# Kernel tuning notes

Measured on AMD Instinct MI355X. Metric: run time of the kernel, lower is better.

Reference implementation:

```python
import jax, jax.numpy as jnp
import numpy as np

N_NODES = 50_000
N_EDGES = 1_600_000
IN_HIDDEN = 256
OUT_HIDDEN = 32
EDGE_HIDDEN = 64
NHEAD = 4
N_EDGE_TYPES = 8
NEG_SLOPE = 0.2


def _glorot(key, shape):
    stdv = np.sqrt(6.0 / (shape[-2] + shape[-1]))
    return jax.random.uniform(key, shape, jnp.float32, -stdv, stdv)


def setup_inputs() -> dict:
    key = jax.random.key(0)
    ks = jax.random.split(key, 10)
    src = jax.random.randint(ks[0], (N_EDGES,), 0, N_NODES, dtype=jnp.int32)
    trg = jax.random.randint(ks[1], (N_EDGES,), 0, N_NODES, dtype=jnp.int32)
    etype = jax.random.randint(ks[2], (N_EDGES,), 0, N_EDGE_TYPES, dtype=jnp.int32)
    edge = jnp.stack([src, trg, etype], axis=0)  # [3, E]
    x = jax.random.normal(ks[3], (N_NODES, IN_HIDDEN), jnp.float32)
    return {
        "edge": edge,
        "x": x,
        "edge_emb": _glorot(ks[4], (N_EDGE_TYPES, EDGE_HIDDEN)),
        "W": _glorot(ks[5], (IN_HIDDEN, OUT_HIDDEN * NHEAD)),
        "W_e": _glorot(ks[6], (EDGE_HIDDEN, EDGE_HIDDEN * NHEAD)),
        "a_l": _glorot(ks[7], (1, NHEAD, OUT_HIDDEN)),
        "a_r": _glorot(ks[8], (1, NHEAD, OUT_HIDDEN)),
        "a_e": _glorot(ks[9], (1, NHEAD, EDGE_HIDDEN)),
    }


def reference(edge, x, edge_emb, W, W_e, a_l, a_r, a_e):
    num_nodes = x.shape[0]
    src, trg, etype = edge[0], edge[1], edge[2]

    # node / edge-type projections
    h = (x @ W).reshape(num_nodes, NHEAD, OUT_HIDDEN)          # [N, H, D]
    h = jnp.where(jnp.isnan(h), 0.0, h)
    e = (edge_emb @ W_e).reshape(N_EDGE_TYPES, NHEAD, EDGE_HIDDEN)  # [T, H, De]

    # per-node / per-type attention logits, gathered to edges -> [E, H]
    h_l = (a_l * h).sum(-1)[src]
    h_r = (a_r * h).sum(-1)[trg]
    h_e = (a_e * e).sum(-1)[etype]
    scores = jax.nn.leaky_relu(h_l + h_r + h_e, NEG_SLOPE)     # [E, H]

    # neighborhood-aware softmax (global max shift, as in original)
    exp_scores = jnp.exp(scores - jnp.max(scores))
    denom = jax.ops.segment_sum(exp_scores, trg, num_segments=num_nodes)  # [N, H]
    attn = (exp_scores / (denom[trg] + 1e-16))[:, :, None]     # [E, H, 1]

    # weighted aggregation: scatter-add messages to targets
    msgs = h[src] * attn                                       # [E, H, D]
    out = jax.ops.segment_sum(msgs, trg, num_segments=num_nodes)  # [N, H, D]
    return out, attn
```

## Files before the change

### kernel.cpp

```cpp
#include <hip/hip_runtime.h>
#include <hip/hip_bf16.h>
#include <hip/hip_fp16.h>

#define N_NODES 50000
#define N_EDGES 1600000
#define IN_H 256
#define NHEAD 4
#define EDGE_H 64
#define N_ET 8


typedef __attribute__((ext_vector_type(8))) short bf16x8v;
typedef __attribute__((ext_vector_type(4))) float f32x4;

__device__ __forceinline__ float ldT(const float* p) { return *p; }
__device__ __forceinline__ float ldT(const __hip_bfloat16* p) { return __bfloat162float(*p); }
__device__ __forceinline__ void stT(float* p, float v) { *p = v; }
__device__ __forceinline__ void stT(__hip_bfloat16* p, float v) { *p = __float2bfloat16(v); }

__device__ __forceinline__ short f2bs(float f) {
    __hip_bfloat16 b = __float2bfloat16(f);
    return (short)__builtin_bit_cast(unsigned short, b);
}
__device__ __forceinline__ float bs2f(short s) {
    return __uint_as_float(((unsigned)(unsigned short)s) << 16);
}

__device__ __forceinline__ unsigned enc_f32(float f) {
    unsigned u = __float_as_uint(f);
    return (u & 0x80000000u) ? ~u : (u | 0x80000000u);
}
__device__ __forceinline__ float dec_f32(unsigned u) {
    return __uint_as_float((u & 0x80000000u) ? (u & 0x7fffffffu) : ~u);
}
__device__ __forceinline__ float lrelu(float v) { return v > 0.f ? v : 0.2f * v; }

__device__ __forceinline__ unsigned pack_h2(float a, float b) {
    unsigned lo = (unsigned)__half_as_ushort(__float2half(a));
    unsigned hi = (unsigned)__half_as_ushort(__float2half(b));
    return lo | (hi << 16);
}
__device__ __forceinline__ float2 unpack_h2(int w) {
    __half2 h = __builtin_bit_cast(__half2, w);
    return __half22float2(h);
}

__global__ void k_detect(const unsigned* __restrict__ xw, int* __restrict__ flag) {
    int lane = threadIdx.x;
    int cnt = 0;
    for (int i = lane; i < 1024; i += 64) {
        unsigned e = (xw[i] >> 23) & 255u;
        if (e >= 64u && e <= 160u) cnt++;
    }
    for (int off = 32; off; off >>= 1) cnt += __shfl_xor(cnt, off);
    if (lane == 0) *flag = (cnt > 512) ? 1 : 0;
}

template<typename T, int EXPECT>
__global__ __launch_bounds__(256) void k_setup(
        const void* __restrict__ Wv, const void* __restrict__ embv,
        const void* __restrict__ Wev, const void* __restrict__ aev,
        __hip_bfloat16* __restrict__ Wt, float* __restrict__ h_e,
        unsigned* __restrict__ hemax, const int* __restrict__ flag) {
    if (*flag != EXPECT) return;
    const T* W   = (const T*)Wv;
    const T* emb = (const T*)embv;
    const T* We  = (const T*)Wev;
    const T* ae  = (const T*)aev;
    if (blockIdx.x == 0) {
        for (int i = threadIdx.x; i < 128 * 256; i += 256) {
            int c = i >> 8, k = i & 255;
            Wt[i] = __float2bfloat16(ldT(W + k * 128 + c));
        }
        return;
    }
    int ty = blockIdx.x - 1;
    int t = threadIdx.x, lane = t & 63;
    float acc = 0.f;
    for (int k = 0; k < EDGE_H; ++k)
        acc += ldT(emb + ty * EDGE_H + k) * ldT(We + k * 256 + t);
    float v = ldT(ae + t) * acc;
    for (int off = 32; off; off >>= 1) v += __shfl_xor(v, off);
    if (lane == 0) {
        h_e[ty * NHEAD + (t >> 6)] = v;
        atomicMax(&hemax[t >> 6], enc_f32(v));
    }
}

template<typename T, int EXPECT>
__global__ __launch_bounds__(256) void k_proj(const void* __restrict__ xv,
        const __hip_bfloat16* __restrict__ Wt, __hip_bfloat16* __restrict__ h,
        float* __restrict__ hl, float* __restrict__ hr,
        const void* __restrict__ alv, const void* __restrict__ arv,
        const int* __restrict__ edge, int* __restrict__ counts,
        const int* __restrict__ flag) {
    if (*flag != EXPECT) return;
    {
        int base = blockIdx.x * 1024;
        int lim = min(base + 1024, N_EDGES);
        for (int i = base + threadIdx.x; i < lim; i += 256)
            atomicAdd(&counts[edge[N_EDGES + i]], 1);
    }
    const T* x  = (const T*)xv;
    const T* al = (const T*)alv;
    const T* ar = (const T*)arv;
    int wid = threadIdx.x >> 6, lane = threadIdx.x & 63;
    int rg = blockIdx.x * 2 + (wid >> 1);
    if (rg >= 3125) return;
    int toff = (wid & 1) * 4;
    int r0 = rg * 16;
    int r = lane & 15;
    int kb = (lane >> 4) * 8;
    const T* xrow = x + (size_t)(r0 + r) * IN_H;
    f32x4 z = {0.f, 0.f, 0.f, 0.f};
    f32x4 acc[4];
#pragma unroll
    for (int t = 0; t < 4; ++t) acc[t] = z;
#pragma unroll
    for (int kk = 0; kk < 8; ++kk) {
        int k0 = kk * 32 + kb;
        bf16x8v a;
        if constexpr (sizeof(T) == 4) {
            float4 lo = *(const float4*)(xrow + k0);
            float4 hi = *(const float4*)(xrow + k0 + 4);
            a[0] = f2bs(lo.x); a[1] = f2bs(lo.y); a[2] = f2bs(lo.z); a[3] = f2bs(lo.w);
            a[4] = f2bs(hi.x); a[5] = f2bs(hi.y); a[6] = f2bs(hi.z); a[7] = f2bs(hi.w);
        } else {
            a = *(const bf16x8v*)(xrow + k0);
        }
#pragma unroll
        for (int t = 0; t < 4; ++t) {
            bf16x8v b = *(const bf16x8v*)(Wt + ((toff + t) * 16 + r) * 256 + k0);
            acc[t] = __builtin_amdgcn_mfma_f32_16x16x32_bf16(a, b, acc[t], 0, 0, 0);
        }
    }
    float alc[4], arc[4];
#pragma unroll
    for (int t = 0; t < 4; ++t) {
        alc[t] = ldT(al + (toff + t) * 16 + r);
        arc[t] = ldT(ar + (toff + t) * 16 + r);
    }
    int ob = (lane >> 4) * 4;
    float pl[2][4] = {{0,0,0,0},{0,0,0,0}}, pr[2][4] = {{0,0,0,0},{0,0,0,0}};
#pragma unroll
    for (int t = 0; t < 4; ++t) {
        int col = (toff + t) * 16 + r;
#pragma unroll
        for (int g = 0; g < 4; ++g) {
            float v = acc[t][g];
            if (v != v) v = 0.f;
            h[(size_t)(r0 + ob + g) * 128 + col] = __float2bfloat16(v);
            pl[t >> 1][g] += alc[t] * v;
            pr[t >> 1][g] += arc[t] * v;
        }
    }
#pragma unroll
    for (int hh = 0; hh < 2; ++hh)
#pragma unroll
        for (int g = 0; g < 4; ++g) {
            float vl = pl[hh][g], vr = pr[hh][g];
#pragma unroll
            for (int off = 8; off; off >>= 1) {
                vl += __shfl_xor(vl, off);
                vr += __shfl_xor(vr, off);
            }
            if (r == 0) {
                int node = r0 + ob + g;
                hl[node * 4 + (toff >> 1) + hh] = vl;
                hr[node * 4 + (toff >> 1) + hh] = vr;
            }
        }
}

__global__ __launch_bounds__(256) void k_maxred(
        const float* __restrict__ hl, unsigned* __restrict__ hlmax) {
    const float NEG = -3.4e38f;
    float4 ml = {NEG, NEG, NEG, NEG};
    for (int n = blockIdx.x * 256 + threadIdx.x; n < N_NODES; n += 128 * 256) {
        float4 a = *(const float4*)(hl + n * 4);
        ml.x = fmaxf(ml.x, a.x); ml.y = fmaxf(ml.y, a.y);
        ml.z = fmaxf(ml.z, a.z); ml.w = fmaxf(ml.w, a.w);
    }
#pragma unroll
    for (int off = 32; off; off >>= 1) {
        ml.x = fmaxf(ml.x, __shfl_xor(ml.x, off));
        ml.y = fmaxf(ml.y, __shfl_xor(ml.y, off));
        ml.z = fmaxf(ml.z, __shfl_xor(ml.z, off));
        ml.w = fmaxf(ml.w, __shfl_xor(ml.w, off));
    }
    if ((threadIdx.x & 63) == 0) {
        atomicMax(&hlmax[0], enc_f32(ml.x)); atomicMax(&hlmax[1], enc_f32(ml.y));
        atomicMax(&hlmax[2], enc_f32(ml.z)); atomicMax(&hlmax[3], enc_f32(ml.w));
    }
}

__global__ __launch_bounds__(1024) void k_scan(
        const int* __restrict__ counts, int* __restrict__ offsets) {
    __shared__ int psum[1024];
    int t = threadIdx.x;
    const int CHUNK = 52;
    int start = t * CHUNK;
    int end = min(start + CHUNK, N_NODES);
    int s = 0;
    for (int i = start; i < end; i += 4) {
        int4 c = *(const int4*)(counts + i);
        s += c.x + c.y + c.z + c.w;
    }
    psum[t] = s;
    __syncthreads();
    for (int off = 1; off < 1024; off <<= 1) {
        int v = (t >= off) ? psum[t - off] : 0;
        __syncthreads();
        psum[t] += v;
        __syncthreads();
    }
    int run = (t == 0) ? 0 : psum[t - 1];
    for (int i = start; i < end; i += 4) {
        int4 c = *(const int4*)(counts + i);
        int4 o;
        o.x = run; o.y = run + c.x; o.z = o.y + c.y; o.w = o.z + c.z;
        *(int4*)(offsets + i) = o;
        run = o.w + c.w;
    }
    if (start < N_NODES && end == N_NODES) offsets[N_NODES] = run;
}

__global__ __launch_bounds__(256) void k_build(
        const int* __restrict__ edge, const int* __restrict__ offsets,
        int* __restrict__ cursor,
        const float* __restrict__ hl, const float* __restrict__ hr,
        const float* __restrict__ he,
        const unsigned* __restrict__ hlmax, const unsigned* __restrict__ hemax,
        int* __restrict__ rec) {
    float G0 = dec_f32(hlmax[0]) + dec_f32(hemax[0]);
    float G1 = dec_f32(hlmax[1]) + dec_f32(hemax[1]);
    float G2 = dec_f32(hlmax[2]) + dec_f32(hemax[2]);
    float G3 = dec_f32(hlmax[3]) + dec_f32(hemax[3]);
    int e = blockIdx.x * 256 + threadIdx.x;
    int s = edge[e], t = edge[N_EDGES + e], ty = edge[2 * N_EDGES + e];
    int pos = offsets[t] + atomicAdd(&cursor[t], 1);
    float4 a = *(const float4*)(hl + s * 4);
    float4 b = *(const float4*)(hr + t * 4);
    float4 c = *(const float4*)(he + ty * 4);
    float p0 = __expf(lrelu(a.x + b.x + c.x) - lrelu(G0 + b.x));
    float p1 = __expf(lrelu(a.y + b.y + c.y) - lrelu(G1 + b.y));
    float p2 = __expf(lrelu(a.z + b.z + c.z) - lrelu(G2 + b.z));
    float p3 = __expf(lrelu(a.w + b.w + c.w) - lrelu(G3 + b.w));
    int4 w;
    w.x = (int)pack_h2(p0, p1);
    w.y = (int)pack_h2(p2, p3);
    w.z = s;
    w.w = e;
    *(int4*)(rec + (size_t)pos * 4) = w;
}

template<typename OUTT, int EXPECT>
__global__ __launch_bounds__(256) void k_agg(
        const int* __restrict__ rec, const int* __restrict__ offsets,
        const __hip_bfloat16* __restrict__ h, void* __restrict__ outv,
        const int* __restrict__ flag) {
    if (*flag != EXPECT) return;
    OUTT* out = (OUTT*)outv;
    int node = (blockIdx.x << 2) + (threadIdx.x >> 6);
    if (node >= N_NODES) return;
    int lane = threadIdx.x & 63;
    int beg = offsets[node], end = offsets[node + 1];

    float d0 = 0.f, d1 = 0.f, d2 = 0.f, d3 = 0.f;
    for (int j = beg + lane; j < end; j += 64) {
        int2 w = *(const int2*)(rec + (size_t)j * 4);
        float2 f01 = unpack_h2(w.x);
        float2 f23 = unpack_h2(w.y);
        d0 += f01.x; d1 += f01.y; d2 += f23.x; d3 += f23.y;
    }
#pragma unroll
    for (int off = 32; off; off >>= 1) {
        d0 += __shfl_xor(d0, off); d1 += __shfl_xor(d1, off);
        d2 += __shfl_xor(d2, off); d3 += __shfl_xor(d3, off);
    }
    float inv0 = 1.f / (d0 + 1e-16f), inv1 = 1.f / (d1 + 1e-16f);
    float inv2 = 1.f / (d2 + 1e-16f), inv3 = 1.f / (d3 + 1e-16f);

    int sub = lane >> 4;
    int l16 = lane & 15;
    int hd  = l16 >> 2;
    float invd = hd == 0 ? inv0 : hd == 1 ? inv1 : hd == 2 ? inv2 : inv3;
    float inva = l16 == 0 ? inv0 : l16 == 1 ? inv1 : l16 == 2 ? inv2 : inv3;
    OUTT* attn_out = out + (size_t)N_NODES * 128;

    float acc[8] = {0.f, 0.f, 0.f, 0.f, 0.f, 0.f, 0.f, 0.f};
    for (int jg = beg; jg < end; jg += 4) {
        int j = jg + sub;
        bool valid = j < end;
        int jc = valid ? j : end - 1;
        int4 w = *(const int4*)(rec + (size_t)jc * 4);
        float2 f01 = unpack_h2(w.x);
        float2 f23 = unpack_h2(w.y);
        int s = w.z;
        if (valid && l16 < 4) {
            float ph = l16 == 0 ? f01.x : l16 == 1 ? f01.y : l16 == 2 ? f23.x : f23.y;
            stT(&attn_out[(size_t)w.w * 4 + l16], ph * inva);
        }
        float phd = hd == 0 ? f01.x : hd == 1 ? f01.y : hd == 2 ? f23.x : f23.y;
        float wgt = valid ? phd * invd : 0.f;
        bf16x8v hv = *(const bf16x8v*)(h + (size_t)s * 128 + l16 * 8);
#pragma unroll
        for (int i = 0; i < 8; ++i) acc[i] += bs2f(hv[i]) * wgt;
    }
#pragma unroll
    for (int i = 0; i < 8; ++i) {
        acc[i] += __shfl_xor(acc[i], 16);
        acc[i] += __shfl_xor(acc[i], 32);
    }
    if (sub == 0) {
#pragma unroll
        for (int i = 0; i < 8; ++i)
            stT(&out[(size_t)node * 128 + l16 * 8 + i], acc[i]);
    }
}

extern "C" void kernel_launch(void* const* d_in, const int* in_sizes, int n_in,
                              void* d_out, int out_size, void* d_ws, size_t ws_size,
                              hipStream_t stream) {
    const int* edge = (const int*)d_in[0];
    const void* x   = d_in[1];
    const void* emb = d_in[2];
    const void* W   = d_in[3];
    const void* We  = d_in[4];
    const void* al  = d_in[5];
    const void* ar  = d_in[6];
    const void* ae  = d_in[7];

    float* ws = (float*)d_ws;
    int* counts     = (int*)ws;
    int* cursor     = counts + 50000;
    unsigned* hlmax = (unsigned*)(counts + 100000);
    unsigned* hemax = hlmax + 8;
    int* flag       = counts + 100012;
    float* hl       = ws + 100064;
    float* hr       = ws + 300064;
    int* offsets    = (int*)ws + 500064;
    float* he       = ws + 550112;
    __hip_bfloat16* Wt = (__hip_bfloat16*)(ws + 550144);
    int* rec        = (int*)ws + 566528;
    __hip_bfloat16* h = (__hip_bfloat16*)(ws + 6966528);

    hipMemsetAsync(ws, 0, (size_t)100064 * 4, stream);

    k_detect<<<1, 64, 0, stream>>>((const unsigned*)x, flag);

    k_setup<float, 1><<<1 + N_ET, 256, 0, stream>>>(W, emb, We, ae, Wt, he,
                                                    hemax, flag);
    k_setup<__hip_bfloat16, 0><<<1 + N_ET, 256, 0, stream>>>(W, emb, We, ae, Wt,
                                                             he, hemax, flag);

    k_proj<float, 1><<<1563, 256, 0, stream>>>(x, Wt, h, hl, hr, al, ar,
                                               edge, counts, flag);
    k_proj<__hip_bfloat16, 0><<<1563, 256, 0, stream>>>(x, Wt, h, hl, hr,
                                                        al, ar, edge, counts, flag);

    k_maxred<<<128, 256, 0, stream>>>(hl, hlmax);
    k_scan<<<1, 1024, 0, stream>>>(counts, offsets);
    k_build<<<6250, 256, 0, stream>>>(edge, offsets, cursor, hl, hr, he,
                                      hlmax, hemax, rec);

    k_agg<float, 1><<<12500, 256, 0, stream>>>(rec, offsets, h, d_out, flag);
    k_agg<__hip_bfloat16, 0><<<12500, 256, 0, stream>>>(rec, offsets, h,
                                                        d_out, flag);
}
```

Baseline: 446.1 us.

## Privatize per-node edge counters into eight copies to cut atomic contention

Edge counting and CSR slot assignment now use eight private counter/cursor arrays selected by block index, and the scan produces per-copy offsets. The aim is to spread atomics on hot target nodes across more addresses. The build kernel now handles 1024 edges per block so the copy mapping matches the counting pass. In exchange the memset grows eightfold, the single-block scan reads eight times more data and does scalar stores, and more scattered memory is touched.

```diff
diff --git a/kernel.cpp b/kernel.cpp
--- a/kernel.cpp
+++ b/kernel.cpp
@@ -92,14 +92,16 @@
         const __hip_bfloat16* __restrict__ Wt, __hip_bfloat16* __restrict__ h,
         float* __restrict__ hl, float* __restrict__ hr,
         const void* __restrict__ alv, const void* __restrict__ arv,
-        const int* __restrict__ edge, int* __restrict__ counts,
+        const int* __restrict__ edge, int* __restrict__ counts8,
         const int* __restrict__ flag) {
     if (*flag != EXPECT) return;
     {
+        int q = blockIdx.x & 7;
         int base = blockIdx.x * 1024;
         int lim = min(base + 1024, N_EDGES);
+        int* cnt = counts8 + q * 50000;
         for (int i = base + threadIdx.x; i < lim; i += 256)
-            atomicAdd(&counts[edge[N_EDGES + i]], 1);
+            atomicAdd(&cnt[edge[N_EDGES + i]], 1);
     }
     const T* x  = (const T*)xv;
     const T* al = (const T*)alv;
@@ -195,17 +197,19 @@
 }
 
 __global__ __launch_bounds__(1024) void k_scan(
-        const int* __restrict__ counts, int* __restrict__ offsets) {
+        const int* __restrict__ counts8, int* __restrict__ offsets,
+        int* __restrict__ off8) {
     __shared__ int psum[1024];
     int t = threadIdx.x;
     const int CHUNK = 52;
     int start = t * CHUNK;
     int end = min(start + CHUNK, N_NODES);
     int s = 0;
-    for (int i = start; i < end; i += 4) {
-        int4 c = *(const int4*)(counts + i);
-        s += c.x + c.y + c.z + c.w;
-    }
+    for (int q = 0; q < 8; ++q)
+        for (int i = start; i < end; i += 4) {
+            int4 c = *(const int4*)(counts8 + q * 50000 + i);
+            s += c.x + c.y + c.z + c.w;
+        }
     psum[t] = s;
     __syncthreads();
     for (int off = 1; off < 1024; off <<= 1) {
@@ -215,19 +219,22 @@
         __syncthreads();
     }
     int run = (t == 0) ? 0 : psum[t - 1];
-    for (int i = start; i < end; i += 4) {
-        int4 c = *(const int4*)(counts + i);
-        int4 o;
-        o.x = run; o.y = run + c.x; o.z = o.y + c.y; o.w = o.z + c.z;
-        *(int4*)(offsets + i) = o;
-        run = o.w + c.w;
+    for (int i = start; i < end; ++i) {
+        offsets[i] = run;
+        int base = run;
+#pragma unroll
+        for (int q = 0; q < 8; ++q) {
+            off8[q * 50000 + i] = base;
+            base += counts8[q * 50000 + i];
+        }
+        run = base;
     }
     if (start < N_NODES && end == N_NODES) offsets[N_NODES] = run;
 }
 
 __global__ __launch_bounds__(256) void k_build(
-        const int* __restrict__ edge, const int* __restrict__ offsets,
-        int* __restrict__ cursor,
+        const int* __restrict__ edge, const int* __restrict__ off8,
+        int* __restrict__ cursor8,
         const float* __restrict__ hl, const float* __restrict__ hr,
         const float* __restrict__ he,
         const unsigned* __restrict__ hlmax, const unsigned* __restrict__ hemax,
@@ -236,22 +243,28 @@
     float G1 = dec_f32(hlmax[1]) + dec_f32(hemax[1]);
     float G2 = dec_f32(hlmax[2]) + dec_f32(hemax[2]);
     float G3 = dec_f32(hlmax[3]) + dec_f32(hemax[3]);
-    int e = blockIdx.x * 256 + threadIdx.x;
-    int s = edge[e], t = edge[N_EDGES + e], ty = edge[2 * N_EDGES + e];
-    int pos = offsets[t] + atomicAdd(&cursor[t], 1);
-    float4 a = *(const float4*)(hl + s * 4);
-    float4 b = *(const float4*)(hr + t * 4);
-    float4 c = *(const float4*)(he + ty * 4);
-    float p0 = __expf(lrelu(a.x + b.x + c.x) - lrelu(G0 + b.x));
-    float p1 = __expf(lrelu(a.y + b.y + c.y) - lrelu(G1 + b.y));
-    float p2 = __expf(lrelu(a.z + b.z + c.z) - lrelu(G2 + b.z));
-    float p3 = __expf(lrelu(a.w + b.w + c.w) - lrelu(G3 + b.w));
-    int4 w;
-    w.x = (int)pack_h2(p0, p1);
-    w.y = (int)pack_h2(p2, p3);
-    w.z = s;
-    w.w = e;
-    *(int4*)(rec + (size_t)pos * 4) = w;
+    int q = blockIdx.x & 7;
+    const int* offq = off8 + q * 50000;
+    int* curq = cursor8 + q * 50000;
+    int base = blockIdx.x * 1024;
+    int lim = min(base + 1024, N_EDGES);
+    for (int e = base + threadIdx.x; e < lim; e += 256) {
+        int s = edge[e], t = edge[N_EDGES + e], ty = edge[2 * N_EDGES + e];
+        int pos = offq[t] + atomicAdd(&curq[t], 1);
+        float4 a = *(const float4*)(hl + s * 4);
+        float4 b = *(const float4*)(hr + t * 4);
+        float4 c = *(const float4*)(he + ty * 4);
+        float p0 = __expf(lrelu(a.x + b.x + c.x) - lrelu(G0 + b.x));
+        float p1 = __expf(lrelu(a.y + b.y + c.y) - lrelu(G1 + b.y));
+        float p2 = __expf(lrelu(a.z + b.z + c.z) - lrelu(G2 + b.z));
+        float p3 = __expf(lrelu(a.w + b.w + c.w) - lrelu(G3 + b.w));
+        int4 w;
+        w.x = (int)pack_h2(p0, p1);
+        w.y = (int)pack_h2(p2, p3);
+        w.z = s;
+        w.w = e;
+        *(int4*)(rec + (size_t)pos * 4) = w;
+    }
 }
 
 template<typename OUTT, int EXPECT>
@@ -332,20 +345,22 @@
     const void* ae  = d_in[7];
 
     float* ws = (float*)d_ws;
-    int* counts     = (int*)ws;
-    int* cursor     = counts + 50000;
-    unsigned* hlmax = (unsigned*)(counts + 100000);
-    unsigned* hemax = hlmax + 8;
-    int* flag       = counts + 100012;
-    float* hl       = ws + 100064;
-    float* hr       = ws + 300064;
-    int* offsets    = (int*)ws + 500064;
-    float* he       = ws + 550112;
-    __hip_bfloat16* Wt = (__hip_bfloat16*)(ws + 550144);
-    int* rec        = (int*)ws + 566528;
-    __hip_bfloat16* h = (__hip_bfloat16*)(ws + 6966528);
-
-    hipMemsetAsync(ws, 0, (size_t)100064 * 4, stream);
+    int* counts8    = (int*)ws;
+    int* cursor8    = counts8 + 400000;
+    unsigned* hlmax = (unsigned*)(counts8 + 800000);
+    unsigned* hemax = hlmax + 2;
+    hemax           = (unsigned*)(counts8 + 800008);
+    int* flag       = counts8 + 800012;
+    float* hl       = ws + 800064;
+    float* hr       = ws + 1000064;
+    int* offsets    = (int*)ws + 1200064;
+    int* off8       = (int*)ws + 1250112;
+    float* he       = ws + 1650112;
+    __hip_bfloat16* Wt = (__hip_bfloat16*)(ws + 1650144);
+    int* rec        = (int*)ws + 1666528;
+    __hip_bfloat16* h = (__hip_bfloat16*)(ws + 8066528);
+
+    hipMemsetAsync(ws, 0, (size_t)800064 * 4, stream);
 
     k_detect<<<1, 64, 0, stream>>>((const unsigned*)x, flag);
 
@@ -355,13 +370,13 @@
                                                              he, hemax, flag);
 
     k_proj<float, 1><<<1563, 256, 0, stream>>>(x, Wt, h, hl, hr, al, ar,
-                                               edge, counts, flag);
+                                               edge, counts8, flag);
     k_proj<__hip_bfloat16, 0><<<1563, 256, 0, stream>>>(x, Wt, h, hl, hr,
-                                                        al, ar, edge, counts, flag);
+                                                        al, ar, edge, counts8, flag);
 
     k_maxred<<<128, 256, 0, stream>>>(hl, hlmax);
-    k_scan<<<1, 1024, 0, stream>>>(counts, offsets);
-    k_build<<<6250, 256, 0, stream>>>(edge, offsets, cursor, hl, hr, he,
+    k_scan<<<1, 1024, 0, stream>>>(counts8, offsets, off8);
+    k_build<<<1563, 256, 0, stream>>>(edge, off8, cursor8, hl, hr, he,
                                       hlmax, hemax, rec);
 
     k_agg<float, 1><<<12500, 256, 0, stream>>>(rec, offsets, h, d_out, flag);
```

Measured after the change: 915.1 us. +105.2%, slower.
